# Kernel optimization log

Hardware: AMD Instinct MI355X
Metric: run time of the kernel (lower is better)

Reference implementation:

```python
import jax, jax.numpy as jnp
import numpy as np

FEATURE_DIM = 256
NUM_HASHES = 128
NUM_NODES = 500000
NUM_SEGMENTS = 512


def setup_inputs() -> dict:
    key = jax.random.key(0)
    k_x, k_b, k_h = jax.random.split(key, 3)
    x = jax.random.normal(k_x, (NUM_NODES, FEATURE_DIM), dtype=jnp.float32)
    batch = jnp.sort(jax.random.randint(k_b, (NUM_NODES,), 0, NUM_SEGMENTS, dtype=jnp.int64))
    hash_matrices = jax.random.normal(k_h, (NUM_HASHES, FEATURE_DIM), dtype=jnp.float32)
    return {"x": x, "batch": batch, "num_segments": NUM_SEGMENTS, "hash_matrices": hash_matrices}


def reference(x, batch, num_segments, hash_matrices):
    # hash_values: [num_nodes, num_hashes]
    hash_values = jnp.matmul(x, hash_matrices.T)
    # per-graph (segment) min over nodes -> [num_segments, num_hashes]
    sketch = jax.ops.segment_min(hash_values, batch, num_segments=num_segments)
    # torch leaves empty groups at zero; empty segments come back +inf here
    sketch = jnp.where(jnp.isinf(sketch), jnp.zeros_like(sketch), sketch)
    return sketch
```

## Files before the change

### kernel.cpp

```cpp
#include <hip/hip_runtime.h>


#define M_NODES 500000
#define KDIM    256
#define NHASH   128
#define NSEG    512

#define BM     128
#define BK     32
#define NCHUNK (KDIM / BK)

typedef __attribute__((ext_vector_type(8))) short bf16x8;
typedef __attribute__((ext_vector_type(4))) float f32x4;

__device__ __forceinline__ unsigned short f2bf(float f) {
    unsigned int u = __float_as_uint(f);
    u += 0x7FFFu + ((u >> 16) & 1u);
    return (unsigned short)(u >> 16);
}
__device__ __forceinline__ float bf2f(unsigned short s) {
    return __uint_as_float(((unsigned int)s) << 16);
}
__device__ __forceinline__ unsigned int enc_f(float f) {
    unsigned int b = __float_as_uint(f);
    return (b & 0x80000000u) ? ~b : (b | 0x80000000u);
}

__device__ __forceinline__ void split8(const float4& A, const float4& B,
                                       bf16x8& hi, bf16x8& lo) {
    const unsigned short h0 = f2bf(A.x), h1 = f2bf(A.y), h2 = f2bf(A.z), h3 = f2bf(A.w);
    const unsigned short h4 = f2bf(B.x), h5 = f2bf(B.y), h6 = f2bf(B.z), h7 = f2bf(B.w);
    hi = (bf16x8){(short)h0, (short)h1, (short)h2, (short)h3,
                  (short)h4, (short)h5, (short)h6, (short)h7};
    lo = (bf16x8){(short)f2bf(A.x - bf2f(h0)), (short)f2bf(A.y - bf2f(h1)),
                  (short)f2bf(A.z - bf2f(h2)), (short)f2bf(A.w - bf2f(h3)),
                  (short)f2bf(B.x - bf2f(h4)), (short)f2bf(B.y - bf2f(h5)),
                  (short)f2bf(B.z - bf2f(h6)), (short)f2bf(B.w - bf2f(h7))};
}

__global__ void hsplit(const float* __restrict__ H,
                       unsigned short* __restrict__ b1f,
                       unsigned short* __restrict__ b2f) {
    const int t = blockIdx.x * 256 + threadIdx.x;
    const int n = t >> 8;
    const int k = t & 255;
    const float h = H[t];
    const unsigned short s1 = f2bf(h);
    const unsigned short s2 = f2bf(h - bf2f(s1));
    const int idx = ((k >> 5) * 8 + (n >> 4)) * 512 + (((k >> 3) & 3) * 16 + (n & 15)) * 8 + (k & 7);
    b1f[idx] = s1;
    b2f[idx] = s2;
}

__global__ __launch_bounds__(256, 3)
void minhash_main(const float* __restrict__ x,
                  const unsigned int* __restrict__ batch_raw,
                  const unsigned short* __restrict__ b1f,
                  const unsigned short* __restrict__ b2f,
                  unsigned int* __restrict__ ws) {
    __shared__ __align__(16) float sc[8448];

    const int tid  = threadIdx.x;
    const int lane = tid & 63;
    const int w    = __builtin_amdgcn_readfirstlane(tid >> 6);
    const int quad = lane >> 4;
    const int c16  = lane & 15;
    const long long blockBase = (long long)blockIdx.x * BM;

    const long long r0 = blockBase + w * 32 + c16;
    const long long r1 = r0 + 16;
    const bool g0 = r0 < (long long)M_NODES;
    const bool g1 = r1 < (long long)M_NODES;
    const float* pa0 = x + r0 * KDIM + quad * 8;
    const float* pa1 = x + r1 * KDIM + quad * 8;

    f32x4 acc[2][8];
    #pragma unroll
    for (int rt = 0; rt < 2; ++rt)
        #pragma unroll
        for (int nt = 0; nt < 8; ++nt)
            acc[rt][nt] = (f32x4){0.f, 0.f, 0.f, 0.f};

    const float4 z4 = make_float4(0.f, 0.f, 0.f, 0.f);
    float4 n0a = g0 ? *(const float4*)(pa0)     : z4;
    float4 n0b = g0 ? *(const float4*)(pa0 + 4) : z4;
    float4 n1a = g1 ? *(const float4*)(pa1)     : z4;
    float4 n1b = g1 ? *(const float4*)(pa1 + 4) : z4;

    const unsigned short* gb1 = b1f + lane * 8;
    const unsigned short* gb2 = b2f + lane * 8;

    for (int chunk = 0; chunk < NCHUNK; ++chunk) {
        const float4 c0a = n0a, c0b = n0b, c1a = n1a, c1b = n1b;
        if (chunk < NCHUNK - 1) {
            const int o = (chunk + 1) * BK;
            n0a = g0 ? *(const float4*)(pa0 + o)     : z4;
            n0b = g0 ? *(const float4*)(pa0 + o + 4) : z4;
            n1a = g1 ? *(const float4*)(pa1 + o)     : z4;
            n1b = g1 ? *(const float4*)(pa1 + o + 4) : z4;
        }
        bf16x8 a1_0, a2_0, a1_1, a2_1;
        split8(c0a, c0b, a1_0, a2_0);
        split8(c1a, c1b, a1_1, a2_1);

        const unsigned short* cb1 = gb1 + chunk * 4096;
        const unsigned short* cb2 = gb2 + chunk * 4096;
        #pragma unroll
        for (int nt = 0; nt < 8; ++nt) {
            const bf16x8 b1v = *(const bf16x8*)(cb1 + nt * 512);
            const bf16x8 b2v = *(const bf16x8*)(cb2 + nt * 512);
            acc[0][nt] = __builtin_amdgcn_mfma_f32_16x16x32_bf16(a1_0, b1v, acc[0][nt], 0, 0, 0);
            acc[0][nt] = __builtin_amdgcn_mfma_f32_16x16x32_bf16(a2_0, b1v, acc[0][nt], 0, 0, 0);
            acc[0][nt] = __builtin_amdgcn_mfma_f32_16x16x32_bf16(a1_0, b2v, acc[0][nt], 0, 0, 0);
            acc[0][nt] = __builtin_amdgcn_mfma_f32_16x16x32_bf16(a2_0, b2v, acc[0][nt], 0, 0, 0);
            acc[1][nt] = __builtin_amdgcn_mfma_f32_16x16x32_bf16(a1_1, b1v, acc[1][nt], 0, 0, 0);
            acc[1][nt] = __builtin_amdgcn_mfma_f32_16x16x32_bf16(a2_1, b1v, acc[1][nt], 0, 0, 0);
            acc[1][nt] = __builtin_amdgcn_mfma_f32_16x16x32_bf16(a1_1, b2v, acc[1][nt], 0, 0, 0);
            acc[1][nt] = __builtin_amdgcn_mfma_f32_16x16x32_bf16(a2_1, b2v, acc[1][nt], 0, 0, 0);
        }
    }

    const bool is64 = (batch_raw[499999] == 0u);
    const long long* bb64 = (const long long*)batch_raw;
    const int*       bb32 = (const int*)batch_raw;

    const int p = lane;
    const int cg = w;
    const long long gn0 = blockBase + 2 * p;
    const long long gn1 = gn0 + 1;
    int seg0 = -1, seg1 = -1;
    if (gn0 < (long long)M_NODES) seg0 = is64 ? (int)bb64[gn0] : bb32[gn0];
    if (gn1 < (long long)M_NODES) seg1 = is64 ? (int)bb64[gn1] : bb32[gn1];

    #pragma unroll
    for (int h = 0; h < 2; ++h) {
        #pragma unroll
        for (int ct = 0; ct < 4; ++ct) {
            #pragma unroll
            for (int rt = 0; rt < 2; ++rt) {
                const int node = w * 32 + rt * 16 + quad * 4;
                const int colp = ct * 16 + c16;
                *(f32x4*)(sc + colp * 132 + node) = acc[rt][h * 4 + ct];
            }
        }
        __syncthreads();

        float v[16];
        int seg;
        if (seg0 == seg1) {
            seg = seg0;
            #pragma unroll
            for (int j = 0; j < 16; ++j) {
                const float2 nv = *(const float2*)(sc + (cg * 16 + j) * 132 + 2 * p);
                v[j] = fminf(nv.x, nv.y);
            }
        } else {
            seg = seg1;
            #pragma unroll
            for (int j = 0; j < 16; ++j) {
                const float2 nv = *(const float2*)(sc + (cg * 16 + j) * 132 + 2 * p);
                if (seg0 >= 0)
                    atomicMin(&ws[seg0 * NHASH + h * 64 + cg * 16 + j], enc_f(nv.x));
                v[j] = nv.y;
            }
        }
        #pragma unroll
        for (int d = 1; d < 64; d <<= 1) {
            const int  oseg = __shfl_down(seg, d, 64);
            const bool ok   = (lane + d < 64) && (oseg == seg);
            #pragma unroll
            for (int j = 0; j < 16; ++j) {
                const float ov = __shfl_down(v[j], d, 64);
                if (ok) v[j] = fminf(v[j], ov);
            }
        }
        const int pseg = __shfl_up(seg, 1, 64);
        if (seg >= 0 && (lane == 0 || pseg != seg)) {
            #pragma unroll
            for (int j = 0; j < 16; ++j)
                atomicMin(&ws[seg * NHASH + h * 64 + cg * 16 + j], enc_f(v[j]));
        }
        __syncthreads();
    }
}

__global__ void minhash_finalize(const unsigned int* __restrict__ ws,
                                 float* __restrict__ out) {
    const int i = blockIdx.x * blockDim.x + threadIdx.x;
    if (i < NSEG * NHASH) {
        const unsigned int u = ws[i];
        out[i] = (u == 0xFFFFFFFFu)
                     ? 0.0f
                     : ((u & 0x80000000u) ? __uint_as_float(u ^ 0x80000000u)
                                          : __uint_as_float(~u));
    }
}

extern "C" void kernel_launch(void* const* d_in, const int* in_sizes, int n_in,
                              void* d_out, int out_size, void* d_ws, size_t ws_size,
                              hipStream_t stream) {
    const float* x = (const float*)d_in[0];
    const unsigned int* batch = (const unsigned int*)d_in[1];
    const float* H = (const float*)d_in[3];

    unsigned int*   ws  = (unsigned int*)d_ws;
    unsigned short* b1f = (unsigned short*)((char*)d_ws + 256 * 1024);
    unsigned short* b2f = (unsigned short*)((char*)d_ws + 320 * 1024);

    hipMemsetAsync(d_ws, 0xFF, NSEG * NHASH * sizeof(unsigned int), stream);
    hsplit<<<(KDIM * NHASH) / 256, 256, 0, stream>>>(H, b1f, b2f);

    const int grid = (M_NODES + BM - 1) / BM;
    minhash_main<<<grid, 256, 0, stream>>>(x, batch, b1f, b2f, ws);
    minhash_finalize<<<(NSEG * NHASH + 255) / 256, 256, 0, stream>>>(ws, (float*)d_out);
}
```

Measured before the change: 750.3 us.

## Halve block row tile to 64 nodes to cut registers and raise occupancy

The block now covers 64 nodes instead of 128, so each wave computes one 16-row MFMA tile instead of two. This halves the accumulator registers and shared scratch, which allows a higher launch-bounds occupancy target and full unrolling of the chunk loop. The epilogue is simplified to one node per lane, dropping the two-node pre-reduction and its extra atomics. In exchange, every block reloads the full B split matrices for half as much work and twice as many blocks issue segment atomics, and each B fragment now feeds fewer MFMAs.

```diff
diff --git a/kernel.cpp b/kernel.cpp
--- a/kernel.cpp
+++ b/kernel.cpp
@@ -6,7 +6,7 @@
 #define NHASH   128
 #define NSEG    512
 
-#define BM     128
+#define BM     64
 #define BK     32
 #define NCHUNK (KDIM / BK)
 
@@ -52,13 +52,13 @@
     b2f[idx] = s2;
 }
 
-__global__ __launch_bounds__(256, 3)
+__global__ __launch_bounds__(256, 4)
 void minhash_main(const float* __restrict__ x,
                   const unsigned int* __restrict__ batch_raw,
                   const unsigned short* __restrict__ b1f,
                   const unsigned short* __restrict__ b2f,
                   unsigned int* __restrict__ ws) {
-    __shared__ __align__(16) float sc[8448];
+    __shared__ __align__(16) float sc[64 * 68];
 
     const int tid  = threadIdx.x;
     const int lane = tid & 63;
@@ -67,41 +67,32 @@
     const int c16  = lane & 15;
     const long long blockBase = (long long)blockIdx.x * BM;
 
-    const long long r0 = blockBase + w * 32 + c16;
-    const long long r1 = r0 + 16;
+    const long long r0 = blockBase + w * 16 + c16;
     const bool g0 = r0 < (long long)M_NODES;
-    const bool g1 = r1 < (long long)M_NODES;
     const float* pa0 = x + r0 * KDIM + quad * 8;
-    const float* pa1 = x + r1 * KDIM + quad * 8;
 
-    f32x4 acc[2][8];
+    f32x4 acc[8];
     #pragma unroll
-    for (int rt = 0; rt < 2; ++rt)
-        #pragma unroll
-        for (int nt = 0; nt < 8; ++nt)
-            acc[rt][nt] = (f32x4){0.f, 0.f, 0.f, 0.f};
+    for (int nt = 0; nt < 8; ++nt)
+        acc[nt] = (f32x4){0.f, 0.f, 0.f, 0.f};
 
     const float4 z4 = make_float4(0.f, 0.f, 0.f, 0.f);
     float4 n0a = g0 ? *(const float4*)(pa0)     : z4;
     float4 n0b = g0 ? *(const float4*)(pa0 + 4) : z4;
-    float4 n1a = g1 ? *(const float4*)(pa1)     : z4;
-    float4 n1b = g1 ? *(const float4*)(pa1 + 4) : z4;
 
     const unsigned short* gb1 = b1f + lane * 8;
     const unsigned short* gb2 = b2f + lane * 8;
 
+    #pragma unroll
     for (int chunk = 0; chunk < NCHUNK; ++chunk) {
-        const float4 c0a = n0a, c0b = n0b, c1a = n1a, c1b = n1b;
+        const float4 c0a = n0a, c0b = n0b;
         if (chunk < NCHUNK - 1) {
             const int o = (chunk + 1) * BK;
             n0a = g0 ? *(const float4*)(pa0 + o)     : z4;
             n0b = g0 ? *(const float4*)(pa0 + o + 4) : z4;
-            n1a = g1 ? *(const float4*)(pa1 + o)     : z4;
-            n1b = g1 ? *(const float4*)(pa1 + o + 4) : z4;
         }
-        bf16x8 a1_0, a2_0, a1_1, a2_1;
-        split8(c0a, c0b, a1_0, a2_0);
-        split8(c1a, c1b, a1_1, a2_1);
+        bf16x8 a1, a2;
+        split8(c0a, c0b, a1, a2);
 
         const unsigned short* cb1 = gb1 + chunk * 4096;
         const unsigned short* cb2 = gb2 + chunk * 4096;
@@ -109,14 +100,10 @@
         for (int nt = 0; nt < 8; ++nt) {
             const bf16x8 b1v = *(const bf16x8*)(cb1 + nt * 512);
             const bf16x8 b2v = *(const bf16x8*)(cb2 + nt * 512);
-            acc[0][nt] = __builtin_amdgcn_mfma_f32_16x16x32_bf16(a1_0, b1v, acc[0][nt], 0, 0, 0);
-            acc[0][nt] = __builtin_amdgcn_mfma_f32_16x16x32_bf16(a2_0, b1v, acc[0][nt], 0, 0, 0);
-            acc[0][nt] = __builtin_amdgcn_mfma_f32_16x16x32_bf16(a1_0, b2v, acc[0][nt], 0, 0, 0);
-            acc[0][nt] = __builtin_amdgcn_mfma_f32_16x16x32_bf16(a2_0, b2v, acc[0][nt], 0, 0, 0);
-            acc[1][nt] = __builtin_amdgcn_mfma_f32_16x16x32_bf16(a1_1, b1v, acc[1][nt], 0, 0, 0);
-            acc[1][nt] = __builtin_amdgcn_mfma_f32_16x16x32_bf16(a2_1, b1v, acc[1][nt], 0, 0, 0);
-            acc[1][nt] = __builtin_amdgcn_mfma_f32_16x16x32_bf16(a1_1, b2v, acc[1][nt], 0, 0, 0);
-            acc[1][nt] = __builtin_amdgcn_mfma_f32_16x16x32_bf16(a2_1, b2v, acc[1][nt], 0, 0, 0);
+            acc[nt] = __builtin_amdgcn_mfma_f32_16x16x32_bf16(a1, b1v, acc[nt], 0, 0, 0);
+            acc[nt] = __builtin_amdgcn_mfma_f32_16x16x32_bf16(a2, b1v, acc[nt], 0, 0, 0);
+            acc[nt] = __builtin_amdgcn_mfma_f32_16x16x32_bf16(a1, b2v, acc[nt], 0, 0, 0);
+            acc[nt] = __builtin_amdgcn_mfma_f32_16x16x32_bf16(a2, b2v, acc[nt], 0, 0, 0);
         }
     }
 
@@ -124,46 +111,25 @@
     const long long* bb64 = (const long long*)batch_raw;
     const int*       bb32 = (const int*)batch_raw;
 
-    const int p = lane;
-    const int cg = w;
-    const long long gn0 = blockBase + 2 * p;
-    const long long gn1 = gn0 + 1;
-    int seg0 = -1, seg1 = -1;
-    if (gn0 < (long long)M_NODES) seg0 = is64 ? (int)bb64[gn0] : bb32[gn0];
-    if (gn1 < (long long)M_NODES) seg1 = is64 ? (int)bb64[gn1] : bb32[gn1];
+    const long long gn = blockBase + lane;
+    int seg = -1;
+    if (gn < (long long)M_NODES) seg = is64 ? (int)bb64[gn] : bb32[gn];
 
     #pragma unroll
     for (int h = 0; h < 2; ++h) {
         #pragma unroll
         for (int ct = 0; ct < 4; ++ct) {
-            #pragma unroll
-            for (int rt = 0; rt < 2; ++rt) {
-                const int node = w * 32 + rt * 16 + quad * 4;
-                const int colp = ct * 16 + c16;
-                *(f32x4*)(sc + colp * 132 + node) = acc[rt][h * 4 + ct];
-            }
+            const int colp = ct * 16 + c16;
+            const int node = w * 16 + quad * 4;
+            *(f32x4*)(sc + colp * 68 + node) = acc[h * 4 + ct];
         }
         __syncthreads();
 
         float v[16];
-        int seg;
-        if (seg0 == seg1) {
-            seg = seg0;
-            #pragma unroll
-            for (int j = 0; j < 16; ++j) {
-                const float2 nv = *(const float2*)(sc + (cg * 16 + j) * 132 + 2 * p);
-                v[j] = fminf(nv.x, nv.y);
-            }
-        } else {
-            seg = seg1;
-            #pragma unroll
-            for (int j = 0; j < 16; ++j) {
-                const float2 nv = *(const float2*)(sc + (cg * 16 + j) * 132 + 2 * p);
-                if (seg0 >= 0)
-                    atomicMin(&ws[seg0 * NHASH + h * 64 + cg * 16 + j], enc_f(nv.x));
-                v[j] = nv.y;
-            }
-        }
+        #pragma unroll
+        for (int j = 0; j < 16; ++j)
+            v[j] = sc[(w * 16 + j) * 68 + lane];
+
         #pragma unroll
         for (int d = 1; d < 64; d <<= 1) {
             const int  oseg = __shfl_down(seg, d, 64);
@@ -178,7 +144,7 @@
         if (seg >= 0 && (lane == 0 || pseg != seg)) {
             #pragma unroll
             for (int j = 0; j < 16; ++j)
-                atomicMin(&ws[seg * NHASH + h * 64 + cg * 16 + j], enc_f(v[j]));
+                atomicMin(&ws[seg * NHASH + h * 64 + w * 16 + j], enc_f(v[j]));
         }
         __syncthreads();
     }
```

Measured after the change: 873.2 us. +16.4%, slower.
